# Performance work log

Measured on AMD Instinct MI355X. Metric: run time of the kernel, lower is better.

Reference implementation:

```python
import jax, jax.numpy as jnp
import numpy as np

# Config mirrors cfg['cluster'] and point_cloud_range from init_kwargs
PCR = np.array([-51.2, -51.2, -5.0, 51.2, 51.2, 3.0], dtype=np.float32)
VOXEL_SIZE = 0.2
SIZE_X = 512  # floor((51.2 - (-51.2)) / 0.2)
EPS = 1.5
MIN_SAMPLES = 5
MIN_P_CLUSTER = 20


def _cluster(points):
    """Faithful jax version of Cluster.forward for batch_size == 1.

    voxel_down_sample -> DBSCAN (euclidean, eps, min_samples) on voxel coords
    -> drop clusters with < MIN_P_CLUSTER voxels -> scatter labels back to points.
    """
    N = points.shape[0]
    # --- voxel_down_sample ---
    coords = jnp.floor((points[:, 1:3] - PCR[:2]) / VOXEL_SIZE).astype(jnp.int32)  # (N,2) x,y
    merged = coords[:, 1] * SIZE_X + coords[:, 0]
    # static-size unique: padded entries get fill_value=-1 at the end
    uniq, inv = jnp.unique(merged, size=N, fill_value=-1, return_inverse=True)
    valid = uniq >= 0  # (N,) real voxels
    vox = jnp.stack([uniq % SIZE_X, uniq // SIZE_X], axis=1).astype(jnp.float32)  # (N,2)

    # --- DBSCAN on voxel coords ---
    d2 = jnp.sum((vox[:, None, :] - vox[None, :, :]) ** 2, axis=-1)  # (N,N)
    adj = (d2 <= EPS * EPS) & valid[:, None] & valid[None, :]  # includes self-edge
    core = (jnp.sum(adj, axis=1) >= MIN_SAMPLES) & valid  # sklearn counts self

    BIG = N  # sentinel > any label
    labels0 = jnp.where(core, jnp.arange(N), BIG)
    adj_core = adj & core[None, :]

    def min_core_neighbor(labels):
        return jnp.min(jnp.where(adj_core, labels[None, :], BIG), axis=1)

    def body(carry):
        labels, _ = carry
        new = jnp.where(core, jnp.minimum(labels, min_core_neighbor(labels)), labels)
        return new, jnp.any(new != labels)

    # min-label propagation = connected components over core-core eps graph
    labels, _ = jax.lax.while_loop(lambda c: c[1], body, (labels0, jnp.array(True)))

    # border points attach to a neighboring core cluster; otherwise noise (-1)
    nb = min_core_neighbor(labels)
    raw = jnp.where(core, labels, jnp.where(valid & (nb < BIG), nb, -1))  # root-id or -1

    # relabel root-ids to consecutive 0..k-1 (sklearn numbering by smallest core idx)
    roots = jnp.unique(raw, size=N, fill_value=BIG)  # sorted; BIG padding at end
    pos = jnp.searchsorted(roots, raw)
    dense = pos - (roots[0] == -1).astype(pos.dtype)
    dense = jnp.where(raw >= 0, dense, -1)

    # drop small clusters (by voxel count), keep remaining ids unchanged
    counts = jnp.zeros(N, jnp.int32).at[jnp.where(dense >= 0, dense, 0)].add(
        jnp.where(dense >= 0, 1, 0))
    keep = counts >= MIN_P_CLUSTER
    final = jnp.where((dense >= 0) & keep[jnp.clip(dense, 0, N - 1)], dense, -1)

    # scatter voxel labels back to points (points_inst_idx has points.dtype, like torch)
    pts_inst = final[inv].astype(points.dtype)
    max_num_inst = jnp.maximum(jnp.max(final) + 1, 0)
    return pts_inst, max_num_inst


def setup_inputs() -> dict:
    key = jax.random.key(0)
    N = 8192
    k1, k2, k3, k4, k5, k6, k7 = jax.random.split(key, 7)
    n_blobs = 64
    centers = jax.random.uniform(k1, (n_blobs, 2), minval=-48.0, maxval=48.0)
    assign = jax.random.randint(k2, (N,), 0, n_blobs)
    xy = centers[assign] + jax.random.normal(k3, (N, 2)) * 1.0
    noise = jax.random.uniform(k4, (N,)) < 0.2
    xy = jnp.where(noise[:, None], jax.random.uniform(k5, (N, 2), minval=-51.0, maxval=51.0), xy)
    xy = jnp.clip(xy, -51.0, 51.0)
    z = jax.random.uniform(k6, (N, 1), minval=-3.0, maxval=1.0)
    feat = jax.random.normal(k7, (N, 1))
    points = jnp.concatenate([jnp.zeros((N, 1)), xy, z, feat], axis=1).astype(jnp.float32)
    return {"points": points, "batch_size": 1}


def reference(points, batch_size):
    # voxel_down_sample asserts batch_size == 1; single-batch path.
    return _cluster(points)
```

## Files before the change

### kernel.cpp

```cpp
#include <hip/hip_runtime.h>
#include <stdint.h>


#define GRIDW 512
#define WPR 16
#define NWORDS 8192
#define NCELLS 262144
#define NONE 0xFFFFFFFFu

#define OFF_OCC    0
#define OFF_CNT    8192
#define OFF_ROOTBM 16384
#define OFF_KEEPBM 16640
#define OFF_CM     16896
#define OFF_LAB    25088
#define OFF_PRE    33280
#define OFF_RPRE   41472

__device__ __forceinline__ void hsum(uint32_t l, uint32_t c, uint32_t r,
                                     uint32_t& h0, uint32_t& h1) {
  uint32_t Wb = (c << 1) | (l >> 31);
  uint32_t Eb = (c >> 1) | (r << 31);
  h0 = Wb ^ c ^ Eb;
  h1 = (Wb & c) | (Eb & (Wb ^ c));
}

__device__ __forceinline__ uint32_t ge5(uint32_t a0, uint32_t a1, uint32_t b0,
                                        uint32_t b1, uint32_t c0, uint32_t c1) {
  uint32_t u0 = a0 ^ b0, cy = a0 & b0;
  uint32_t t = a1 ^ b1;
  uint32_t u1 = t ^ cy;
  uint32_t u2 = (a1 & b1) | (cy & t);
  uint32_t v0 = u0 ^ c0, k0 = u0 & c0;
  uint32_t t2 = u1 ^ c1;
  uint32_t v1 = t2 ^ k0;
  uint32_t k1 = (u1 & c1) | (k0 & t2);
  uint32_t v2 = u2 ^ k1;
  uint32_t v3 = u2 & k1;
  return v3 | (v2 & (v1 | v0));
}

__device__ __forceinline__ uint32_t aread(uint32_t* p) {
  return __hip_atomic_load(p, __ATOMIC_RELAXED, __HIP_MEMORY_SCOPE_AGENT);
}

__device__ __forceinline__ uint32_t findc(uint32_t* L, uint32_t x) {
  uint32_t r = x, p = aread(&L[r]);
  while (p != r) { r = p; p = aread(&L[r]); }
  while (x > r) {
    uint32_t nx = aread(&L[x]);
    if (nx <= r) break;
    atomicCAS(&L[x], nx, r);
    x = nx;
  }
  return r;
}

__device__ __forceinline__ void unite(uint32_t* L, uint32_t a, uint32_t b) {
  for (;;) {
    a = findc(L, a);
    b = findc(L, b);
    if (a == b) return;
    uint32_t lo = min(a, b), hi = max(a, b);
    if (atomicCAS(&L[hi], hi, lo) == hi) return;
    a = lo; b = hi;
  }
}

__global__ void k_vox(const float* __restrict__ pts, uint32_t* __restrict__ ws,
                      int npts) {
  int i = blockIdx.x * 256 + threadIdx.x;
  if (i >= npts) return;
  float x = pts[i * 5 + 1];
  float y = pts[i * 5 + 2];
  int cx = (int)floorf((x - (-51.2f)) / 0.2f);
  int cy = (int)floorf((y - (-51.2f)) / 0.2f);
  cx = min(max(cx, 0), GRIDW - 1);
  cy = min(max(cy, 0), GRIDW - 1);
  int cell = cy * GRIDW + cx;
  atomicOr(&ws[OFF_OCC + (cell >> 5)], 1u << (cell & 31));
}

__global__ void k_scan_cm(uint32_t* __restrict__ ws) {
  const uint32_t* occ = ws + OFF_OCC;
  int tid = threadIdx.x;
  if (blockIdx.x == 0) {
    __shared__ uint32_t wsum[4];
    ws[OFF_ROOTBM + tid] = 0u;
    ws[OFF_KEEPBM + tid] = 0u;
    int base = tid * 32;
    uint32_t s = 0;
    for (int j = 0; j < 32; j++) s += __popc(occ[base + j]);
    int lane = tid & 63, wv = tid >> 6;
    uint32_t inc = s;
    for (int d = 1; d < 64; d <<= 1) { uint32_t t = __shfl_up(inc, d); if (lane >= d) inc += t; }
    if (lane == 63) wsum[wv] = inc;
    __syncthreads();
    uint32_t woff = 0;
    for (int k = 0; k < wv; k++) woff += wsum[k];
    uint32_t excl = woff + inc - s;
    uint32_t* pre = ws + OFF_PRE;
    for (int j = 0; j < 32; j++) { pre[base + j] = excl; excl += __popc(occ[base + j]); }
  } else {
    int wi = (blockIdx.x - 1) * 256 + tid;
    ws[OFF_LAB + wi] = (uint32_t)wi;
    ws[OFF_CNT + wi] = 0u;
    uint32_t cB = occ[wi];
    int y = wi >> 4, wx = wi & 15;
    uint32_t lB = wx ? occ[wi - 1] : 0u;
    uint32_t rB = (wx < 15) ? occ[wi + 1] : 0u;
    uint32_t cA = 0, lA = 0, rA = 0, cC = 0, lC = 0, rC = 0;
    if (y > 0) { int wa = wi - WPR; cA = occ[wa]; lA = wx ? occ[wa - 1] : 0u; rA = (wx < 15) ? occ[wa + 1] : 0u; }
    if (y < GRIDW - 1) { int wc = wi + WPR; cC = occ[wc]; lC = wx ? occ[wc - 1] : 0u; rC = (wx < 15) ? occ[wc + 1] : 0u; }
    uint32_t a0, a1, b0, b1, c0, c1;
    hsum(lA, cA, rA, a0, a1); hsum(lB, cB, rB, b0, b1); hsum(lC, cC, rC, c0, c1);
    ws[OFF_CM + wi] = ge5(a0, a1, b0, b1, c0, c1) & cB;
  }
}

__global__ void k_merge(uint32_t* __restrict__ ws) {
  int cell = blockIdx.x * 256 + threadIdx.x;
  const uint32_t* occ = ws + OFF_OCC;
  const uint32_t* cm = ws + OFF_CM;
  const uint32_t* pre = ws + OFF_PRE;
  uint32_t* lab = ws + OFF_LAB;
  int wi = cell >> 5, b = cell & 31, wx = wi & 15;
  uint32_t cw = cm[wi];
  if (!((cw >> b) & 1)) return;
  int y = cell >> 9;
  uint32_t cB = occ[wi];
  int r = pre[wi] + __popc(cB & ((1u << b) - 1u));
  bool eC = (b < 31) ? ((cw >> (b + 1)) & 1) : ((wx < 15) ? (cm[wi + 1] & 1) : false);
  if (eC) unite(lab, r, (b < 31) ? r + 1 : pre[wi + 1]);
  if (y < GRIDW - 1) {
    uint32_t cmS = cm[wi + WPR];
    uint32_t occS = occ[wi + WPR];
    int rS = pre[wi + WPR];
    if ((cmS >> b) & 1) unite(lab, r, rS + __popc(occS & ((1u << b) - 1u)));
    bool seC = (b < 31) ? ((cmS >> (b + 1)) & 1) : ((wx < 15) ? (cm[wi + WPR + 1] & 1) : false);
    if (seC) unite(lab, r, (b < 31) ? rS + __popc(occS & ((2u << b) - 1u)) : pre[wi + WPR + 1]);
    bool swC = (b > 0) ? ((cmS >> (b - 1)) & 1) : ((wx > 0) ? (cm[wi + WPR - 1] >> 31) : false);
    if (swC) unite(lab, r, (b > 0) ? rS + __popc(occS & ((1u << (b - 1)) - 1u)) : rS - 1);
  }
}

__global__ void k_cb(uint32_t* __restrict__ ws) {
  int cell = blockIdx.x * 256 + threadIdx.x;
  int wi = cell >> 5, b = cell & 31, wx = wi & 15;
  const uint32_t* occ = ws + OFF_OCC;
  uint32_t cB = occ[wi];
  if (!((cB >> b) & 1)) return;
  const uint32_t* cm = ws + OFF_CM;
  const uint32_t* pre = ws + OFF_PRE;
  uint32_t* lab = ws + OFF_LAB;
  uint32_t* cnt = ws + OFF_CNT;
  int y = cell >> 9;
  uint32_t cw = cm[wi];
  int r = pre[wi] + __popc(cB & ((1u << b) - 1u));
  if ((cw >> b) & 1) {
    uint32_t root = findc(lab, r);
    lab[r] = root;
    if (root == (uint32_t)r) atomicOr(&ws[OFF_ROOTBM + (r >> 5)], 1u << (r & 31));
    atomicAdd(&cnt[root], 1u);
  } else {
    uint32_t m = NONE;
    bool wC = (b > 0) ? ((cw >> (b - 1)) & 1) : ((wx > 0) ? (cm[wi - 1] >> 31) : false);
    if (wC) m = min(m, findc(lab, (b > 0) ? r - 1 : (int)pre[wi] - 1));
    bool eC = (b < 31) ? ((cw >> (b + 1)) & 1) : ((wx < 15) ? (cm[wi + 1] & 1) : false);
    if (eC) m = min(m, findc(lab, (b < 31) ? r + 1 : pre[wi + 1]));
    if (y > 0) {
      uint32_t cmN = cm[wi - WPR], occN = occ[wi - WPR];
      int rN = pre[wi - WPR];
      if ((cmN >> b) & 1) m = min(m, findc(lab, rN + __popc(occN & ((1u << b) - 1u))));
      bool neC = (b < 31) ? ((cmN >> (b + 1)) & 1) : ((wx < 15) ? (cm[wi - WPR + 1] & 1) : false);
      if (neC) m = min(m, findc(lab, (b < 31) ? rN + __popc(occN & ((2u << b) - 1u)) : pre[wi - WPR + 1]));
      bool nwC = (b > 0) ? ((cmN >> (b - 1)) & 1) : ((wx > 0) ? (cm[wi - WPR - 1] >> 31) : false);
      if (nwC) m = min(m, findc(lab, (b > 0) ? rN + __popc(occN & ((1u << (b - 1)) - 1u)) : rN - 1));
    }
    if (y < GRIDW - 1) {
      uint32_t cmS = cm[wi + WPR], occS = occ[wi + WPR];
      int rS = pre[wi + WPR];
      if ((cmS >> b) & 1) m = min(m, findc(lab, rS + __popc(occS & ((1u << b) - 1u))));
      bool seC = (b < 31) ? ((cmS >> (b + 1)) & 1) : ((wx < 15) ? (cm[wi + WPR + 1] & 1) : false);
      if (seC) m = min(m, findc(lab, (b < 31) ? rS + __popc(occS & ((2u << b) - 1u)) : pre[wi + WPR + 1]));
      bool swC = (b > 0) ? ((cmS >> (b - 1)) & 1) : ((wx > 0) ? (cm[wi + WPR - 1] >> 31) : false);
      if (swC) m = min(m, findc(lab, (b > 0) ? rS + __popc(occS & ((1u << (b - 1)) - 1u)) : rS - 1));
    }
    lab[r] = m;
    if (m != NONE) atomicAdd(&cnt[m], 1u);
  }
}

__global__ void k_finish(uint32_t* __restrict__ ws, float* __restrict__ out,
                         int npts) {
  int tid = threadIdx.x;
  __shared__ uint32_t wsum[4];
  __shared__ int smax;
  if (tid == 0) smax = -1;
  __syncthreads();
  uint32_t rb = ws[OFF_ROOTBM + tid];
  uint32_t v = __popc(rb);
  int lane = tid & 63, wv = tid >> 6;
  uint32_t inc = v;
  for (int d = 1; d < 64; d <<= 1) { uint32_t t = __shfl_up(inc, d); if (lane >= d) inc += t; }
  if (lane == 63) wsum[wv] = inc;
  __syncthreads();
  uint32_t woff = 0;
  for (int k = 0; k < wv; k++) woff += wsum[k];
  uint32_t excl = woff + inc - v;
  ws[OFF_RPRE + tid] = excl;
  uint32_t keep = 0;
  int mx = -1, d = (int)excl;
  while (rb) {
    int b = __ffs(rb) - 1; rb &= rb - 1;
    int r = tid * 32 + b;
    if (ws[OFF_CNT + r] >= 20u) { keep |= 1u << b; mx = d; }
    d++;
  }
  ws[OFF_KEEPBM + tid] = keep;
  if (mx >= 0) atomicMax(&smax, mx);
  __syncthreads();
  if (tid == 0) out[npts] = (float)(smax + 1);
}

__global__ void k_scatter(const float* __restrict__ pts,
                          const uint32_t* __restrict__ ws,
                          float* __restrict__ out, int npts) {
  int i = blockIdx.x * 256 + threadIdx.x;
  if (i >= npts) return;
  float x = pts[i * 5 + 1];
  float y = pts[i * 5 + 2];
  int cx = (int)floorf((x - (-51.2f)) / 0.2f);
  int cy = (int)floorf((y - (-51.2f)) / 0.2f);
  cx = min(max(cx, 0), GRIDW - 1);
  cy = min(max(cy, 0), GRIDW - 1);
  int cell = cy * GRIDW + cx;
  int wi = cell >> 5;
  int r = ws[OFF_PRE + wi] + __popc(ws[OFF_OCC + wi] & ((1u << (cell & 31)) - 1u));
  uint32_t l = ws[OFF_LAB + r];
  float o = -1.0f;
  if (l != NONE && ((ws[OFF_KEEPBM + (l >> 5)] >> (l & 31)) & 1)) {
    int dnum = ws[OFF_RPRE + (l >> 5)] +
               __popc(ws[OFF_ROOTBM + (l >> 5)] & ((1u << (l & 31)) - 1u));
    o = (float)dnum;
  }
  out[i] = o;
}

extern "C" void kernel_launch(void* const* d_in, const int* in_sizes, int n_in,
                              void* d_out, int out_size, void* d_ws, size_t ws_size,
                              hipStream_t stream) {
  const float* pts = (const float*)d_in[0];
  int npts = in_sizes[0] / 5;
  uint32_t* ws = (uint32_t*)d_ws;
  float* out = (float*)d_out;
  int pblocks = (npts + 255) / 256;
  hipMemsetAsync(d_ws, 0, NWORDS * 4, stream);
  k_vox<<<pblocks, 256, 0, stream>>>(pts, ws, npts);
  k_scan_cm<<<33, 256, 0, stream>>>(ws);
  k_merge<<<NCELLS / 256, 256, 0, stream>>>(ws);
  k_cb<<<NCELLS / 256, 256, 0, stream>>>(ws);
  k_finish<<<1, 256, 0, stream>>>(ws, out, npts);
  k_scatter<<<pblocks, 256, 0, stream>>>(pts, ws, out, npts);
}
```

Before: 96.39 us.

## Fuse all clustering stages into one cooperative kernel with grid syncs

Replaces the memset and six separate kernel launches with a single cooperative kernel of 256 blocks that separates the phases (zeroing, voxelization, core mask and prefix scan, union, border attach, finish, scatter) with grid-wide syncs. Each thread now handles a 4-bit nibble of cells instead of one cell per thread, and the prefix scan is spread across blocks followed by a small block-sum scan. The aim is to remove launch and inter-kernel gaps, in exchange for the cost of about eight grid barriers and a cooperative launch.

```diff
diff --git a/kernel.cpp b/kernel.cpp
--- a/kernel.cpp
+++ b/kernel.cpp
@@ -1,21 +1,28 @@
 #include <hip/hip_runtime.h>
+#include <hip/hip_cooperative_groups.h>
 #include <stdint.h>
+
+namespace cg = cooperative_groups;
 
 
 #define GRIDW 512
 #define WPR 16
 #define NWORDS 8192
-#define NCELLS 262144
+#define NB 256
+#define NT 256
+#define TOT (NB * NT)
 #define NONE 0xFFFFFFFFu
 
 #define OFF_OCC    0
 #define OFF_CNT    8192
 #define OFF_ROOTBM 16384
 #define OFF_KEEPBM 16640
-#define OFF_CM     16896
-#define OFF_LAB    25088
-#define OFF_PRE    33280
-#define OFF_RPRE   41472
+#define ZERO_WORDS 16896
+#define OFF_BSUM   16896
+#define OFF_RPRE   17152
+#define OFF_CM     17408
+#define OFF_LAB    25600
+#define OFF_PRE    33792
 
 __device__ __forceinline__ void hsum(uint32_t l, uint32_t c, uint32_t r,
                                      uint32_t& h0, uint32_t& h1) {
@@ -67,184 +74,198 @@
   }
 }
 
-__global__ void k_vox(const float* __restrict__ pts, uint32_t* __restrict__ ws,
-                      int npts) {
-  int i = blockIdx.x * 256 + threadIdx.x;
-  if (i >= npts) return;
-  float x = pts[i * 5 + 1];
-  float y = pts[i * 5 + 2];
-  int cx = (int)floorf((x - (-51.2f)) / 0.2f);
-  int cy = (int)floorf((y - (-51.2f)) / 0.2f);
-  cx = min(max(cx, 0), GRIDW - 1);
-  cy = min(max(cy, 0), GRIDW - 1);
-  int cell = cy * GRIDW + cx;
-  atomicOr(&ws[OFF_OCC + (cell >> 5)], 1u << (cell & 31));
-}
-
-__global__ void k_scan_cm(uint32_t* __restrict__ ws) {
-  const uint32_t* occ = ws + OFF_OCC;
-  int tid = threadIdx.x;
-  if (blockIdx.x == 0) {
-    __shared__ uint32_t wsum[4];
-    ws[OFF_ROOTBM + tid] = 0u;
-    ws[OFF_KEEPBM + tid] = 0u;
-    int base = tid * 32;
-    uint32_t s = 0;
-    for (int j = 0; j < 32; j++) s += __popc(occ[base + j]);
-    int lane = tid & 63, wv = tid >> 6;
-    uint32_t inc = s;
-    for (int d = 1; d < 64; d <<= 1) { uint32_t t = __shfl_up(inc, d); if (lane >= d) inc += t; }
-    if (lane == 63) wsum[wv] = inc;
-    __syncthreads();
-    uint32_t woff = 0;
-    for (int k = 0; k < wv; k++) woff += wsum[k];
-    uint32_t excl = woff + inc - s;
-    uint32_t* pre = ws + OFF_PRE;
-    for (int j = 0; j < 32; j++) { pre[base + j] = excl; excl += __popc(occ[base + j]); }
-  } else {
-    int wi = (blockIdx.x - 1) * 256 + tid;
-    ws[OFF_LAB + wi] = (uint32_t)wi;
-    ws[OFF_CNT + wi] = 0u;
-    uint32_t cB = occ[wi];
-    int y = wi >> 4, wx = wi & 15;
-    uint32_t lB = wx ? occ[wi - 1] : 0u;
-    uint32_t rB = (wx < 15) ? occ[wi + 1] : 0u;
+__global__ __launch_bounds__(NT) void cluster_ck(const float* __restrict__ pts,
+                                                 float* __restrict__ out,
+                                                 uint32_t* __restrict__ ws,
+                                                 int npts) {
+  cg::grid_group grid = cg::this_grid();
+  const int tid = threadIdx.x;
+  const int gid = blockIdx.x * NT + tid;
+  const int lane = tid & 63, wv = tid >> 6;
+  __shared__ uint32_t wsum[4];
+  __shared__ int smax;
+
+  uint32_t* occ = ws + OFF_OCC;
+  uint32_t* cm = ws + OFF_CM;
+  uint32_t* lab = ws + OFF_LAB;
+  uint32_t* pre = ws + OFF_PRE;
+  uint32_t* cnt = ws + OFF_CNT;
+  uint32_t* bsum = ws + OFF_BSUM;
+
+  if (gid < ZERO_WORDS) ws[gid] = 0u;
+  if (gid < NWORDS) lab[gid] = (uint32_t)gid;
+  grid.sync();
+
+  int myCell = -1;
+  if (gid < npts) {
+    float x = pts[gid * 5 + 1];
+    float y = pts[gid * 5 + 2];
+    int cx = (int)floorf((x - (-51.2f)) / 0.2f);
+    int cy = (int)floorf((y - (-51.2f)) / 0.2f);
+    cx = min(max(cx, 0), GRIDW - 1);
+    cy = min(max(cy, 0), GRIDW - 1);
+    myCell = cy * GRIDW + cx;
+    atomicOr(&occ[myCell >> 5], 1u << (myCell & 31));
+  }
+  grid.sync();
+
+  uint32_t s = 0;
+  if (gid < NWORDS) {
+    uint32_t cB = occ[gid];
+    s = __popc(cB);
+    int y = gid >> 4, wx = gid & 15;
+    uint32_t lB = wx ? occ[gid - 1] : 0u;
+    uint32_t rB = (wx < 15) ? occ[gid + 1] : 0u;
     uint32_t cA = 0, lA = 0, rA = 0, cC = 0, lC = 0, rC = 0;
-    if (y > 0) { int wa = wi - WPR; cA = occ[wa]; lA = wx ? occ[wa - 1] : 0u; rA = (wx < 15) ? occ[wa + 1] : 0u; }
-    if (y < GRIDW - 1) { int wc = wi + WPR; cC = occ[wc]; lC = wx ? occ[wc - 1] : 0u; rC = (wx < 15) ? occ[wc + 1] : 0u; }
+    if (y > 0) { int wa = gid - WPR; cA = occ[wa]; lA = wx ? occ[wa - 1] : 0u; rA = (wx < 15) ? occ[wa + 1] : 0u; }
+    if (y < GRIDW - 1) { int wc = gid + WPR; cC = occ[wc]; lC = wx ? occ[wc - 1] : 0u; rC = (wx < 15) ? occ[wc + 1] : 0u; }
     uint32_t a0, a1, b0, b1, c0, c1;
     hsum(lA, cA, rA, a0, a1); hsum(lB, cB, rB, b0, b1); hsum(lC, cC, rC, c0, c1);
-    ws[OFF_CM + wi] = ge5(a0, a1, b0, b1, c0, c1) & cB;
-  }
-}
-
-__global__ void k_merge(uint32_t* __restrict__ ws) {
-  int cell = blockIdx.x * 256 + threadIdx.x;
-  const uint32_t* occ = ws + OFF_OCC;
-  const uint32_t* cm = ws + OFF_CM;
-  const uint32_t* pre = ws + OFF_PRE;
-  uint32_t* lab = ws + OFF_LAB;
-  int wi = cell >> 5, b = cell & 31, wx = wi & 15;
-  uint32_t cw = cm[wi];
-  if (!((cw >> b) & 1)) return;
-  int y = cell >> 9;
-  uint32_t cB = occ[wi];
-  int r = pre[wi] + __popc(cB & ((1u << b) - 1u));
-  bool eC = (b < 31) ? ((cw >> (b + 1)) & 1) : ((wx < 15) ? (cm[wi + 1] & 1) : false);
-  if (eC) unite(lab, r, (b < 31) ? r + 1 : pre[wi + 1]);
-  if (y < GRIDW - 1) {
-    uint32_t cmS = cm[wi + WPR];
-    uint32_t occS = occ[wi + WPR];
-    int rS = pre[wi + WPR];
-    if ((cmS >> b) & 1) unite(lab, r, rS + __popc(occS & ((1u << b) - 1u)));
-    bool seC = (b < 31) ? ((cmS >> (b + 1)) & 1) : ((wx < 15) ? (cm[wi + WPR + 1] & 1) : false);
-    if (seC) unite(lab, r, (b < 31) ? rS + __popc(occS & ((2u << b) - 1u)) : pre[wi + WPR + 1]);
-    bool swC = (b > 0) ? ((cmS >> (b - 1)) & 1) : ((wx > 0) ? (cm[wi + WPR - 1] >> 31) : false);
-    if (swC) unite(lab, r, (b > 0) ? rS + __popc(occS & ((1u << (b - 1)) - 1u)) : rS - 1);
-  }
-}
-
-__global__ void k_cb(uint32_t* __restrict__ ws) {
-  int cell = blockIdx.x * 256 + threadIdx.x;
-  int wi = cell >> 5, b = cell & 31, wx = wi & 15;
-  const uint32_t* occ = ws + OFF_OCC;
-  uint32_t cB = occ[wi];
-  if (!((cB >> b) & 1)) return;
-  const uint32_t* cm = ws + OFF_CM;
-  const uint32_t* pre = ws + OFF_PRE;
-  uint32_t* lab = ws + OFF_LAB;
-  uint32_t* cnt = ws + OFF_CNT;
-  int y = cell >> 9;
-  uint32_t cw = cm[wi];
-  int r = pre[wi] + __popc(cB & ((1u << b) - 1u));
-  if ((cw >> b) & 1) {
-    uint32_t root = findc(lab, r);
-    lab[r] = root;
-    if (root == (uint32_t)r) atomicOr(&ws[OFF_ROOTBM + (r >> 5)], 1u << (r & 31));
-    atomicAdd(&cnt[root], 1u);
-  } else {
-    uint32_t m = NONE;
-    bool wC = (b > 0) ? ((cw >> (b - 1)) & 1) : ((wx > 0) ? (cm[wi - 1] >> 31) : false);
-    if (wC) m = min(m, findc(lab, (b > 0) ? r - 1 : (int)pre[wi] - 1));
-    bool eC = (b < 31) ? ((cw >> (b + 1)) & 1) : ((wx < 15) ? (cm[wi + 1] & 1) : false);
-    if (eC) m = min(m, findc(lab, (b < 31) ? r + 1 : pre[wi + 1]));
-    if (y > 0) {
-      uint32_t cmN = cm[wi - WPR], occN = occ[wi - WPR];
-      int rN = pre[wi - WPR];
-      if ((cmN >> b) & 1) m = min(m, findc(lab, rN + __popc(occN & ((1u << b) - 1u))));
-      bool neC = (b < 31) ? ((cmN >> (b + 1)) & 1) : ((wx < 15) ? (cm[wi - WPR + 1] & 1) : false);
-      if (neC) m = min(m, findc(lab, (b < 31) ? rN + __popc(occN & ((2u << b) - 1u)) : pre[wi - WPR + 1]));
-      bool nwC = (b > 0) ? ((cmN >> (b - 1)) & 1) : ((wx > 0) ? (cm[wi - WPR - 1] >> 31) : false);
-      if (nwC) m = min(m, findc(lab, (b > 0) ? rN + __popc(occN & ((1u << (b - 1)) - 1u)) : rN - 1));
-    }
-    if (y < GRIDW - 1) {
-      uint32_t cmS = cm[wi + WPR], occS = occ[wi + WPR];
-      int rS = pre[wi + WPR];
-      if ((cmS >> b) & 1) m = min(m, findc(lab, rS + __popc(occS & ((1u << b) - 1u))));
-      bool seC = (b < 31) ? ((cmS >> (b + 1)) & 1) : ((wx < 15) ? (cm[wi + WPR + 1] & 1) : false);
-      if (seC) m = min(m, findc(lab, (b < 31) ? rS + __popc(occS & ((2u << b) - 1u)) : pre[wi + WPR + 1]));
-      bool swC = (b > 0) ? ((cmS >> (b - 1)) & 1) : ((wx > 0) ? (cm[wi + WPR - 1] >> 31) : false);
-      if (swC) m = min(m, findc(lab, (b > 0) ? rS + __popc(occS & ((1u << (b - 1)) - 1u)) : rS - 1));
-    }
-    lab[r] = m;
-    if (m != NONE) atomicAdd(&cnt[m], 1u);
-  }
-}
-
-__global__ void k_finish(uint32_t* __restrict__ ws, float* __restrict__ out,
-                         int npts) {
-  int tid = threadIdx.x;
-  __shared__ uint32_t wsum[4];
-  __shared__ int smax;
-  if (tid == 0) smax = -1;
-  __syncthreads();
-  uint32_t rb = ws[OFF_ROOTBM + tid];
-  uint32_t v = __popc(rb);
-  int lane = tid & 63, wv = tid >> 6;
-  uint32_t inc = v;
+    cm[gid] = ge5(a0, a1, b0, b1, c0, c1) & cB;
+  }
+  uint32_t inc = s;
   for (int d = 1; d < 64; d <<= 1) { uint32_t t = __shfl_up(inc, d); if (lane >= d) inc += t; }
   if (lane == 63) wsum[wv] = inc;
   __syncthreads();
   uint32_t woff = 0;
   for (int k = 0; k < wv; k++) woff += wsum[k];
-  uint32_t excl = woff + inc - v;
-  ws[OFF_RPRE + tid] = excl;
-  uint32_t keep = 0;
-  int mx = -1, d = (int)excl;
-  while (rb) {
-    int b = __ffs(rb) - 1; rb &= rb - 1;
-    int r = tid * 32 + b;
-    if (ws[OFF_CNT + r] >= 20u) { keep |= 1u << b; mx = d; }
-    d++;
-  }
-  ws[OFF_KEEPBM + tid] = keep;
-  if (mx >= 0) atomicMax(&smax, mx);
-  __syncthreads();
-  if (tid == 0) out[npts] = (float)(smax + 1);
-}
-
-__global__ void k_scatter(const float* __restrict__ pts,
-                          const uint32_t* __restrict__ ws,
-                          float* __restrict__ out, int npts) {
-  int i = blockIdx.x * 256 + threadIdx.x;
-  if (i >= npts) return;
-  float x = pts[i * 5 + 1];
-  float y = pts[i * 5 + 2];
-  int cx = (int)floorf((x - (-51.2f)) / 0.2f);
-  int cy = (int)floorf((y - (-51.2f)) / 0.2f);
-  cx = min(max(cx, 0), GRIDW - 1);
-  cy = min(max(cy, 0), GRIDW - 1);
-  int cell = cy * GRIDW + cx;
-  int wi = cell >> 5;
-  int r = ws[OFF_PRE + wi] + __popc(ws[OFF_OCC + wi] & ((1u << (cell & 31)) - 1u));
-  uint32_t l = ws[OFF_LAB + r];
-  float o = -1.0f;
-  if (l != NONE && ((ws[OFF_KEEPBM + (l >> 5)] >> (l & 31)) & 1)) {
-    int dnum = ws[OFF_RPRE + (l >> 5)] +
-               __popc(ws[OFF_ROOTBM + (l >> 5)] & ((1u << (l & 31)) - 1u));
-    o = (float)dnum;
-  }
-  out[i] = o;
+  uint32_t binc = woff + inc;
+  if (tid == NT - 1) bsum[blockIdx.x] = binc;
+  grid.sync();
+
+  if (blockIdx.x == 0 && tid < 32) {
+    uint32_t u = bsum[tid];
+    for (int d = 1; d < 32; d <<= 1) { uint32_t t = __shfl_up(u, d); if (tid >= d) u += t; }
+    bsum[tid] = u;
+  }
+  grid.sync();
+
+  if (gid < NWORDS) {
+    uint32_t off = blockIdx.x ? bsum[blockIdx.x - 1] : 0u;
+    pre[gid] = off + binc - s;
+  }
+  grid.sync();
+
+  {
+    int wi = gid >> 3;
+    uint32_t cw = cm[wi];
+    uint32_t nib = (cw >> ((gid & 7) << 2)) & 0xFu;
+    if (nib) {
+      int wx = wi & 15, y = wi >> 4;
+      uint32_t cB = occ[wi];
+      int rbase = pre[wi];
+      bool hasS = y < GRIDW - 1;
+      uint32_t cmS = hasS ? cm[wi + WPR] : 0u;
+      uint32_t occS = hasS ? occ[wi + WPR] : 0u;
+      int rS = hasS ? (int)pre[wi + WPR] : 0;
+      for (int j = 0; j < 4; j++) {
+        int b = ((gid & 7) << 2) + j;
+        if (!((cw >> b) & 1)) continue;
+        int r = rbase + __popc(cB & ((1u << b) - 1u));
+        bool eC = (b < 31) ? ((cw >> (b + 1)) & 1) : ((wx < 15) ? (cm[wi + 1] & 1) : false);
+        if (eC) unite(lab, r, (b < 31) ? r + 1 : pre[wi + 1]);
+        if (hasS) {
+          if ((cmS >> b) & 1) unite(lab, r, rS + __popc(occS & ((1u << b) - 1u)));
+          bool seC = (b < 31) ? ((cmS >> (b + 1)) & 1) : ((wx < 15) ? (cm[wi + WPR + 1] & 1) : false);
+          if (seC) unite(lab, r, (b < 31) ? rS + __popc(occS & ((2u << b) - 1u)) : pre[wi + WPR + 1]);
+          bool swC = (b > 0) ? ((cmS >> (b - 1)) & 1) : ((wx > 0) ? (cm[wi + WPR - 1] >> 31) : false);
+          if (swC) unite(lab, r, (b > 0) ? rS + __popc(occS & ((1u << (b - 1)) - 1u)) : rS - 1);
+        }
+      }
+    }
+  }
+  grid.sync();
+
+  {
+    int wi = gid >> 3;
+    uint32_t cB = occ[wi];
+    uint32_t nib = (cB >> ((gid & 7) << 2)) & 0xFu;
+    if (nib) {
+      int wx = wi & 15, y = wi >> 4;
+      uint32_t cw = cm[wi];
+      int rbase = pre[wi];
+      bool hasN = y > 0, hasS = y < GRIDW - 1;
+      uint32_t cmN = 0, occN = 0, cmS = 0, occS = 0;
+      int rN = 0, rS = 0;
+      if (hasN) { cmN = cm[wi - WPR]; occN = occ[wi - WPR]; rN = pre[wi - WPR]; }
+      if (hasS) { cmS = cm[wi + WPR]; occS = occ[wi + WPR]; rS = pre[wi + WPR]; }
+      for (int j = 0; j < 4; j++) {
+        int b = ((gid & 7) << 2) + j;
+        if (!((cB >> b) & 1)) continue;
+        int r = rbase + __popc(cB & ((1u << b) - 1u));
+        if ((cw >> b) & 1) {
+          uint32_t root = findc(lab, r);
+          lab[r] = root;
+          if (root == (uint32_t)r) atomicOr(&ws[OFF_ROOTBM + (r >> 5)], 1u << (r & 31));
+          atomicAdd(&cnt[root], 1u);
+        } else {
+          uint32_t m = NONE;
+          bool wC = (b > 0) ? ((cw >> (b - 1)) & 1) : ((wx > 0) ? (cm[wi - 1] >> 31) : false);
+          if (wC) m = min(m, findc(lab, (b > 0) ? r - 1 : rbase - 1));
+          bool eC = (b < 31) ? ((cw >> (b + 1)) & 1) : ((wx < 15) ? (cm[wi + 1] & 1) : false);
+          if (eC) m = min(m, findc(lab, (b < 31) ? r + 1 : pre[wi + 1]));
+          if (hasN) {
+            if ((cmN >> b) & 1) m = min(m, findc(lab, rN + __popc(occN & ((1u << b) - 1u))));
+            bool neC = (b < 31) ? ((cmN >> (b + 1)) & 1) : ((wx < 15) ? (cm[wi - WPR + 1] & 1) : false);
+            if (neC) m = min(m, findc(lab, (b < 31) ? rN + __popc(occN & ((2u << b) - 1u)) : pre[wi - WPR + 1]));
+            bool nwC = (b > 0) ? ((cmN >> (b - 1)) & 1) : ((wx > 0) ? (cm[wi - WPR - 1] >> 31) : false);
+            if (nwC) m = min(m, findc(lab, (b > 0) ? rN + __popc(occN & ((1u << (b - 1)) - 1u)) : rN - 1));
+          }
+          if (hasS) {
+            if ((cmS >> b) & 1) m = min(m, findc(lab, rS + __popc(occS & ((1u << b) - 1u))));
+            bool seC = (b < 31) ? ((cmS >> (b + 1)) & 1) : ((wx < 15) ? (cm[wi + WPR + 1] & 1) : false);
+            if (seC) m = min(m, findc(lab, (b < 31) ? rS + __popc(occS & ((2u << b) - 1u)) : pre[wi + WPR + 1]));
+            bool swC = (b > 0) ? ((cmS >> (b - 1)) & 1) : ((wx > 0) ? (cm[wi + WPR - 1] >> 31) : false);
+            if (swC) m = min(m, findc(lab, (b > 0) ? rS + __popc(occS & ((1u << (b - 1)) - 1u)) : rS - 1));
+          }
+          lab[r] = m;
+          if (m != NONE) atomicAdd(&cnt[m], 1u);
+        }
+      }
+    }
+  }
+  grid.sync();
+
+  if (blockIdx.x == 0) {
+    if (tid == 0) smax = -1;
+    __syncthreads();
+    uint32_t rb = ws[OFF_ROOTBM + tid];
+    uint32_t v = __popc(rb);
+    uint32_t rinc = v;
+    for (int d = 1; d < 64; d <<= 1) { uint32_t t = __shfl_up(rinc, d); if (lane >= d) rinc += t; }
+    if (lane == 63) wsum[wv] = rinc;
+    __syncthreads();
+    uint32_t roff = 0;
+    for (int k = 0; k < wv; k++) roff += wsum[k];
+    uint32_t excl = roff + rinc - v;
+    ws[OFF_RPRE + tid] = excl;
+    uint32_t keep = 0;
+    int mx = -1, d = (int)excl;
+    while (rb) {
+      int b = __ffs(rb) - 1; rb &= rb - 1;
+      int r = tid * 32 + b;
+      if (cnt[r] >= 20u) { keep |= 1u << b; mx = d; }
+      d++;
+    }
+    ws[OFF_KEEPBM + tid] = keep;
+    if (mx >= 0) atomicMax(&smax, mx);
+    __syncthreads();
+    if (tid == 0) out[npts] = (float)(smax + 1);
+  }
+  grid.sync();
+
+  if (gid < npts) {
+    int wi = myCell >> 5;
+    int r = pre[wi] + __popc(occ[wi] & ((1u << (myCell & 31)) - 1u));
+    uint32_t l = lab[r];
+    float o = -1.0f;
+    if (l != NONE && ((ws[OFF_KEEPBM + (l >> 5)] >> (l & 31)) & 1)) {
+      int dnum = ws[OFF_RPRE + (l >> 5)] +
+                 __popc(ws[OFF_ROOTBM + (l >> 5)] & ((1u << (l & 31)) - 1u));
+      o = (float)dnum;
+    }
+    out[gid] = o;
+  }
 }
 
 extern "C" void kernel_launch(void* const* d_in, const int* in_sizes, int n_in,
@@ -254,12 +275,7 @@
   int npts = in_sizes[0] / 5;
   uint32_t* ws = (uint32_t*)d_ws;
   float* out = (float*)d_out;
-  int pblocks = (npts + 255) / 256;
-  hipMemsetAsync(d_ws, 0, NWORDS * 4, stream);
-  k_vox<<<pblocks, 256, 0, stream>>>(pts, ws, npts);
-  k_scan_cm<<<33, 256, 0, stream>>>(ws);
-  k_merge<<<NCELLS / 256, 256, 0, stream>>>(ws);
-  k_cb<<<NCELLS / 256, 256, 0, stream>>>(ws);
-  k_finish<<<1, 256, 0, stream>>>(ws, out, npts);
-  k_scatter<<<pblocks, 256, 0, stream>>>(pts, ws, out, npts);
-}
+  void* args[] = {(void*)&pts, (void*)&out, (void*)&ws, (void*)&npts};
+  hipLaunchCooperativeKernel((void*)cluster_ck, dim3(NB), dim3(NT), args, 0,
+                             stream);
+}
```

Result: slower. 305.5 us (+216.9%).

## Index union-find by grid cell and compute core masks inline, dropping scan kernel

Applied to the files above, without the earlier changes.

Switches the label and count arrays from compacted voxel ranks to direct indexing by grid cell (262144 entries). This removes the prefix-sum/core-mask kernel, and core bits are recomputed from the occupancy bitmap inside the merge and border kernels. The root-bitmap scan in the finish kernel grows to 8192 words processed by one block, and a full-size init kernel replaces the small memset. The intent is to remove one launch and the rank-lookup indirection, at the cost of more init traffic, redundant bit arithmetic, and a longer serial scan.

```diff
diff --git a/kernel.cpp b/kernel.cpp
--- a/kernel.cpp
+++ b/kernel.cpp
@@ -9,13 +9,11 @@
 #define NONE 0xFFFFFFFFu
 
 #define OFF_OCC    0
-#define OFF_CNT    8192
-#define OFF_ROOTBM 16384
-#define OFF_KEEPBM 16640
-#define OFF_CM     16896
-#define OFF_LAB    25088
-#define OFF_PRE    33280
-#define OFF_RPRE   41472
+#define OFF_ROOTBM 8192
+#define OFF_KEEPBM 16384
+#define OFF_RPRE   24576
+#define OFF_LAB    32768
+#define OFF_CNT    294912
 
 __device__ __forceinline__ void hsum(uint32_t l, uint32_t c, uint32_t r,
                                      uint32_t& h0, uint32_t& h1) {
@@ -40,6 +38,24 @@
   return v3 | (v2 & (v1 | v0));
 }
 
+__device__ __forceinline__ uint32_t coreRbit(uint32_t cU, uint32_t rU, uint32_t cM,
+                                             uint32_t rM, uint32_t cD, uint32_t rD) {
+  if (!(rM & 1u)) return 0u;
+  int n = __popc((cU >> 31) | ((rU & 3u) << 1)) +
+          __popc((cM >> 31) | ((rM & 3u) << 1)) +
+          __popc((cD >> 31) | ((rD & 3u) << 1));
+  return n >= 5 ? 1u : 0u;
+}
+
+__device__ __forceinline__ uint32_t coreLbit(uint32_t cU, uint32_t lU, uint32_t cM,
+                                             uint32_t lM, uint32_t cD, uint32_t lD) {
+  if (!(lM >> 31)) return 0u;
+  int n = __popc(((lU >> 30) & 3u) | ((cU & 1u) << 2)) +
+          __popc(((lM >> 30) & 3u) | ((cM & 1u) << 2)) +
+          __popc(((lD >> 30) & 3u) | ((cD & 1u) << 2));
+  return n >= 5 ? 1u : 0u;
+}
+
 __device__ __forceinline__ uint32_t aread(uint32_t* p) {
   return __hip_atomic_load(p, __ATOMIC_RELAXED, __HIP_MEMORY_SCOPE_AGENT);
 }
@@ -65,6 +81,13 @@
     if (atomicCAS(&L[hi], hi, lo) == hi) return;
     a = lo; b = hi;
   }
+}
+
+__global__ void k_init(uint32_t* __restrict__ ws) {
+  int i = blockIdx.x * 256 + threadIdx.x;
+  ws[OFF_LAB + i] = (uint32_t)i;
+  ws[OFF_CNT + i] = 0u;
+  if (i < NWORDS) { ws[OFF_OCC + i] = 0u; ws[OFF_ROOTBM + i] = 0u; }
 }
 
 __global__ void k_vox(const float* __restrict__ pts, uint32_t* __restrict__ ws,
@@ -81,143 +104,124 @@
   atomicOr(&ws[OFF_OCC + (cell >> 5)], 1u << (cell & 31));
 }
 
-__global__ void k_scan_cm(uint32_t* __restrict__ ws) {
-  const uint32_t* occ = ws + OFF_OCC;
-  int tid = threadIdx.x;
-  if (blockIdx.x == 0) {
-    __shared__ uint32_t wsum[4];
-    ws[OFF_ROOTBM + tid] = 0u;
-    ws[OFF_KEEPBM + tid] = 0u;
-    int base = tid * 32;
-    uint32_t s = 0;
-    for (int j = 0; j < 32; j++) s += __popc(occ[base + j]);
-    int lane = tid & 63, wv = tid >> 6;
-    uint32_t inc = s;
-    for (int d = 1; d < 64; d <<= 1) { uint32_t t = __shfl_up(inc, d); if (lane >= d) inc += t; }
-    if (lane == 63) wsum[wv] = inc;
-    __syncthreads();
-    uint32_t woff = 0;
-    for (int k = 0; k < wv; k++) woff += wsum[k];
-    uint32_t excl = woff + inc - s;
-    uint32_t* pre = ws + OFF_PRE;
-    for (int j = 0; j < 32; j++) { pre[base + j] = excl; excl += __popc(occ[base + j]); }
-  } else {
-    int wi = (blockIdx.x - 1) * 256 + tid;
-    ws[OFF_LAB + wi] = (uint32_t)wi;
-    ws[OFF_CNT + wi] = 0u;
-    uint32_t cB = occ[wi];
-    int y = wi >> 4, wx = wi & 15;
-    uint32_t lB = wx ? occ[wi - 1] : 0u;
-    uint32_t rB = (wx < 15) ? occ[wi + 1] : 0u;
-    uint32_t cA = 0, lA = 0, rA = 0, cC = 0, lC = 0, rC = 0;
-    if (y > 0) { int wa = wi - WPR; cA = occ[wa]; lA = wx ? occ[wa - 1] : 0u; rA = (wx < 15) ? occ[wa + 1] : 0u; }
-    if (y < GRIDW - 1) { int wc = wi + WPR; cC = occ[wc]; lC = wx ? occ[wc - 1] : 0u; rC = (wx < 15) ? occ[wc + 1] : 0u; }
-    uint32_t a0, a1, b0, b1, c0, c1;
-    hsum(lA, cA, rA, a0, a1); hsum(lB, cB, rB, b0, b1); hsum(lC, cC, rC, c0, c1);
-    ws[OFF_CM + wi] = ge5(a0, a1, b0, b1, c0, c1) & cB;
-  }
-}
-
 __global__ void k_merge(uint32_t* __restrict__ ws) {
   int cell = blockIdx.x * 256 + threadIdx.x;
   const uint32_t* occ = ws + OFF_OCC;
-  const uint32_t* cm = ws + OFF_CM;
-  const uint32_t* pre = ws + OFF_PRE;
   uint32_t* lab = ws + OFF_LAB;
-  int wi = cell >> 5, b = cell & 31, wx = wi & 15;
-  uint32_t cw = cm[wi];
-  if (!((cw >> b) & 1)) return;
-  int y = cell >> 9;
+  int wi = cell >> 5, b = cell & 31, wx = wi & 15, y = cell >> 9;
   uint32_t cB = occ[wi];
-  int r = pre[wi] + __popc(cB & ((1u << b) - 1u));
-  bool eC = (b < 31) ? ((cw >> (b + 1)) & 1) : ((wx < 15) ? (cm[wi + 1] & 1) : false);
-  if (eC) unite(lab, r, (b < 31) ? r + 1 : pre[wi + 1]);
+  if (!((cB >> b) & 1)) return;
+  uint32_t lB = wx ? occ[wi - 1] : 0u;
+  uint32_t rB = (wx < 15) ? occ[wi + 1] : 0u;
+  uint32_t cA = 0, lA = 0, rA = 0, cC = 0, lC = 0, rC = 0, cD = 0, lD = 0, rD = 0;
+  if (y > 0) { int w = wi - WPR; cA = occ[w]; lA = wx ? occ[w - 1] : 0u; rA = (wx < 15) ? occ[w + 1] : 0u; }
+  if (y < GRIDW - 1) { int w = wi + WPR; cC = occ[w]; lC = wx ? occ[w - 1] : 0u; rC = (wx < 15) ? occ[w + 1] : 0u; }
+  if (y < GRIDW - 2) { int w = wi + 2 * WPR; cD = occ[w]; lD = wx ? occ[w - 1] : 0u; rD = (wx < 15) ? occ[w + 1] : 0u; }
+  uint32_t hA0, hA1, hB0, hB1, hC0, hC1, hD0, hD1;
+  hsum(lA, cA, rA, hA0, hA1); hsum(lB, cB, rB, hB0, hB1);
+  hsum(lC, cC, rC, hC0, hC1); hsum(lD, cD, rD, hD0, hD1);
+  uint32_t cmB = ge5(hA0, hA1, hB0, hB1, hC0, hC1) & cB;
+  if (!((cmB >> b) & 1)) return;
+  bool eC = (b < 31) ? (((cmB >> (b + 1)) & 1) != 0)
+                     : (coreRbit(cA, rA, cB, rB, cC, rC) != 0);
+  if (eC) unite(lab, cell, cell + 1);
   if (y < GRIDW - 1) {
-    uint32_t cmS = cm[wi + WPR];
-    uint32_t occS = occ[wi + WPR];
-    int rS = pre[wi + WPR];
-    if ((cmS >> b) & 1) unite(lab, r, rS + __popc(occS & ((1u << b) - 1u)));
-    bool seC = (b < 31) ? ((cmS >> (b + 1)) & 1) : ((wx < 15) ? (cm[wi + WPR + 1] & 1) : false);
-    if (seC) unite(lab, r, (b < 31) ? rS + __popc(occS & ((2u << b) - 1u)) : pre[wi + WPR + 1]);
-    bool swC = (b > 0) ? ((cmS >> (b - 1)) & 1) : ((wx > 0) ? (cm[wi + WPR - 1] >> 31) : false);
-    if (swC) unite(lab, r, (b > 0) ? rS + __popc(occS & ((1u << (b - 1)) - 1u)) : rS - 1);
+    uint32_t cmS = ge5(hB0, hB1, hC0, hC1, hD0, hD1) & cC;
+    if ((cmS >> b) & 1) unite(lab, cell, cell + GRIDW);
+    bool seC = (b < 31) ? (((cmS >> (b + 1)) & 1) != 0)
+                        : (coreRbit(cB, rB, cC, rC, cD, rD) != 0);
+    if (seC) unite(lab, cell, cell + GRIDW + 1);
+    bool swC = (b > 0) ? (((cmS >> (b - 1)) & 1) != 0)
+                       : (coreLbit(cB, lB, cC, lC, cD, lD) != 0);
+    if (swC) unite(lab, cell, cell + GRIDW - 1);
   }
 }
 
 __global__ void k_cb(uint32_t* __restrict__ ws) {
   int cell = blockIdx.x * 256 + threadIdx.x;
-  int wi = cell >> 5, b = cell & 31, wx = wi & 15;
   const uint32_t* occ = ws + OFF_OCC;
+  uint32_t* lab = ws + OFF_LAB;
+  uint32_t* cnt = ws + OFF_CNT;
+  int wi = cell >> 5, b = cell & 31, wx = wi & 15, y = cell >> 9;
   uint32_t cB = occ[wi];
   if (!((cB >> b) & 1)) return;
-  const uint32_t* cm = ws + OFF_CM;
-  const uint32_t* pre = ws + OFF_PRE;
-  uint32_t* lab = ws + OFF_LAB;
-  uint32_t* cnt = ws + OFF_CNT;
-  int y = cell >> 9;
-  uint32_t cw = cm[wi];
-  int r = pre[wi] + __popc(cB & ((1u << b) - 1u));
-  if ((cw >> b) & 1) {
-    uint32_t root = findc(lab, r);
-    lab[r] = root;
-    if (root == (uint32_t)r) atomicOr(&ws[OFF_ROOTBM + (r >> 5)], 1u << (r & 31));
+  uint32_t lB = wx ? occ[wi - 1] : 0u;
+  uint32_t rB = (wx < 15) ? occ[wi + 1] : 0u;
+  uint32_t cZ = 0, lZ = 0, rZ = 0, cA = 0, lA = 0, rA = 0;
+  uint32_t cC = 0, lC = 0, rC = 0, cD = 0, lD = 0, rD = 0;
+  if (y > 1) { int w = wi - 2 * WPR; cZ = occ[w]; lZ = wx ? occ[w - 1] : 0u; rZ = (wx < 15) ? occ[w + 1] : 0u; }
+  if (y > 0) { int w = wi - WPR; cA = occ[w]; lA = wx ? occ[w - 1] : 0u; rA = (wx < 15) ? occ[w + 1] : 0u; }
+  if (y < GRIDW - 1) { int w = wi + WPR; cC = occ[w]; lC = wx ? occ[w - 1] : 0u; rC = (wx < 15) ? occ[w + 1] : 0u; }
+  if (y < GRIDW - 2) { int w = wi + 2 * WPR; cD = occ[w]; lD = wx ? occ[w - 1] : 0u; rD = (wx < 15) ? occ[w + 1] : 0u; }
+  uint32_t hZ0, hZ1, hA0, hA1, hB0, hB1, hC0, hC1, hD0, hD1;
+  hsum(lZ, cZ, rZ, hZ0, hZ1); hsum(lA, cA, rA, hA0, hA1); hsum(lB, cB, rB, hB0, hB1);
+  hsum(lC, cC, rC, hC0, hC1); hsum(lD, cD, rD, hD0, hD1);
+  uint32_t cw0 = ge5(hA0, hA1, hB0, hB1, hC0, hC1) & cB;
+  if ((cw0 >> b) & 1) {
+    uint32_t root = findc(lab, cell);
+    lab[cell] = root;
+    if (root == (uint32_t)cell) atomicOr(&ws[OFF_ROOTBM + wi], 1u << b);
     atomicAdd(&cnt[root], 1u);
   } else {
+    uint32_t cwm1 = ge5(hZ0, hZ1, hA0, hA1, hB0, hB1) & cA;
+    uint32_t cw1 = ge5(hB0, hB1, hC0, hC1, hD0, hD1) & cC;
     uint32_t m = NONE;
-    bool wC = (b > 0) ? ((cw >> (b - 1)) & 1) : ((wx > 0) ? (cm[wi - 1] >> 31) : false);
-    if (wC) m = min(m, findc(lab, (b > 0) ? r - 1 : (int)pre[wi] - 1));
-    bool eC = (b < 31) ? ((cw >> (b + 1)) & 1) : ((wx < 15) ? (cm[wi + 1] & 1) : false);
-    if (eC) m = min(m, findc(lab, (b < 31) ? r + 1 : pre[wi + 1]));
+    bool t;
+    t = (b > 0) ? (((cw0 >> (b - 1)) & 1) != 0) : (coreLbit(cA, lA, cB, lB, cC, lC) != 0);
+    if (t) m = min(m, findc(lab, cell - 1));
+    t = (b < 31) ? (((cw0 >> (b + 1)) & 1) != 0) : (coreRbit(cA, rA, cB, rB, cC, rC) != 0);
+    if (t) m = min(m, findc(lab, cell + 1));
     if (y > 0) {
-      uint32_t cmN = cm[wi - WPR], occN = occ[wi - WPR];
-      int rN = pre[wi - WPR];
-      if ((cmN >> b) & 1) m = min(m, findc(lab, rN + __popc(occN & ((1u << b) - 1u))));
-      bool neC = (b < 31) ? ((cmN >> (b + 1)) & 1) : ((wx < 15) ? (cm[wi - WPR + 1] & 1) : false);
-      if (neC) m = min(m, findc(lab, (b < 31) ? rN + __popc(occN & ((2u << b) - 1u)) : pre[wi - WPR + 1]));
-      bool nwC = (b > 0) ? ((cmN >> (b - 1)) & 1) : ((wx > 0) ? (cm[wi - WPR - 1] >> 31) : false);
-      if (nwC) m = min(m, findc(lab, (b > 0) ? rN + __popc(occN & ((1u << (b - 1)) - 1u)) : rN - 1));
+      if ((cwm1 >> b) & 1) m = min(m, findc(lab, cell - GRIDW));
+      t = (b > 0) ? (((cwm1 >> (b - 1)) & 1) != 0) : (coreLbit(cZ, lZ, cA, lA, cB, lB) != 0);
+      if (t) m = min(m, findc(lab, cell - GRIDW - 1));
+      t = (b < 31) ? (((cwm1 >> (b + 1)) & 1) != 0) : (coreRbit(cZ, rZ, cA, rA, cB, rB) != 0);
+      if (t) m = min(m, findc(lab, cell - GRIDW + 1));
     }
     if (y < GRIDW - 1) {
-      uint32_t cmS = cm[wi + WPR], occS = occ[wi + WPR];
-      int rS = pre[wi + WPR];
-      if ((cmS >> b) & 1) m = min(m, findc(lab, rS + __popc(occS & ((1u << b) - 1u))));
-      bool seC = (b < 31) ? ((cmS >> (b + 1)) & 1) : ((wx < 15) ? (cm[wi + WPR + 1] & 1) : false);
-      if (seC) m = min(m, findc(lab, (b < 31) ? rS + __popc(occS & ((2u << b) - 1u)) : pre[wi + WPR + 1]));
-      bool swC = (b > 0) ? ((cmS >> (b - 1)) & 1) : ((wx > 0) ? (cm[wi + WPR - 1] >> 31) : false);
-      if (swC) m = min(m, findc(lab, (b > 0) ? rS + __popc(occS & ((1u << (b - 1)) - 1u)) : rS - 1));
-    }
-    lab[r] = m;
+      if ((cw1 >> b) & 1) m = min(m, findc(lab, cell + GRIDW));
+      t = (b > 0) ? (((cw1 >> (b - 1)) & 1) != 0) : (coreLbit(cB, lB, cC, lC, cD, lD) != 0);
+      if (t) m = min(m, findc(lab, cell + GRIDW - 1));
+      t = (b < 31) ? (((cw1 >> (b + 1)) & 1) != 0) : (coreRbit(cB, rB, cC, rC, cD, rD) != 0);
+      if (t) m = min(m, findc(lab, cell + GRIDW + 1));
+    }
+    lab[cell] = m;
     if (m != NONE) atomicAdd(&cnt[m], 1u);
   }
 }
 
 __global__ void k_finish(uint32_t* __restrict__ ws, float* __restrict__ out,
                          int npts) {
-  int tid = threadIdx.x;
   __shared__ uint32_t wsum[4];
   __shared__ int smax;
+  int tid = threadIdx.x;
   if (tid == 0) smax = -1;
-  __syncthreads();
-  uint32_t rb = ws[OFF_ROOTBM + tid];
-  uint32_t v = __popc(rb);
+  int base = tid * 32;
+  uint32_t s = 0;
+  for (int j = 0; j < 32; j++) s += __popc(ws[OFF_ROOTBM + base + j]);
   int lane = tid & 63, wv = tid >> 6;
-  uint32_t inc = v;
+  uint32_t inc = s;
   for (int d = 1; d < 64; d <<= 1) { uint32_t t = __shfl_up(inc, d); if (lane >= d) inc += t; }
   if (lane == 63) wsum[wv] = inc;
   __syncthreads();
   uint32_t woff = 0;
   for (int k = 0; k < wv; k++) woff += wsum[k];
-  uint32_t excl = woff + inc - v;
-  ws[OFF_RPRE + tid] = excl;
-  uint32_t keep = 0;
-  int mx = -1, d = (int)excl;
-  while (rb) {
-    int b = __ffs(rb) - 1; rb &= rb - 1;
-    int r = tid * 32 + b;
-    if (ws[OFF_CNT + r] >= 20u) { keep |= 1u << b; mx = d; }
-    d++;
-  }
-  ws[OFF_KEEPBM + tid] = keep;
+  uint32_t excl = woff + inc - s;
+  int mx = -1;
+  for (int j = 0; j < 32; j++) {
+    uint32_t rbw = ws[OFF_ROOTBM + base + j];
+    ws[OFF_RPRE + base + j] = excl;
+    uint32_t rb = rbw, keep = 0;
+    int d = (int)excl;
+    while (rb) {
+      int b2 = __ffs(rb) - 1; rb &= rb - 1;
+      int r = (base + j) * 32 + b2;
+      if (ws[OFF_CNT + r] >= 20u) { keep |= 1u << b2; mx = d; }
+      d++;
+    }
+    ws[OFF_KEEPBM + base + j] = keep;
+    excl += __popc(rbw);
+  }
   if (mx >= 0) atomicMax(&smax, mx);
   __syncthreads();
   if (tid == 0) out[npts] = (float)(smax + 1);
@@ -235,14 +239,14 @@
   cx = min(max(cx, 0), GRIDW - 1);
   cy = min(max(cy, 0), GRIDW - 1);
   int cell = cy * GRIDW + cx;
-  int wi = cell >> 5;
-  int r = ws[OFF_PRE + wi] + __popc(ws[OFF_OCC + wi] & ((1u << (cell & 31)) - 1u));
-  uint32_t l = ws[OFF_LAB + r];
+  uint32_t l = ws[OFF_LAB + cell];
   float o = -1.0f;
-  if (l != NONE && ((ws[OFF_KEEPBM + (l >> 5)] >> (l & 31)) & 1)) {
-    int dnum = ws[OFF_RPRE + (l >> 5)] +
-               __popc(ws[OFF_ROOTBM + (l >> 5)] & ((1u << (l & 31)) - 1u));
-    o = (float)dnum;
+  if (l != NONE) {
+    if ((ws[OFF_KEEPBM + (l >> 5)] >> (l & 31)) & 1) {
+      int dnum = ws[OFF_RPRE + (l >> 5)] +
+                 __popc(ws[OFF_ROOTBM + (l >> 5)] & ((1u << (l & 31)) - 1u));
+      o = (float)dnum;
+    }
   }
   out[i] = o;
 }
@@ -255,9 +259,8 @@
   uint32_t* ws = (uint32_t*)d_ws;
   float* out = (float*)d_out;
   int pblocks = (npts + 255) / 256;
-  hipMemsetAsync(d_ws, 0, NWORDS * 4, stream);
+  k_init<<<NCELLS / 256, 256, 0, stream>>>(ws);
   k_vox<<<pblocks, 256, 0, stream>>>(pts, ws, npts);
-  k_scan_cm<<<33, 256, 0, stream>>>(ws);
   k_merge<<<NCELLS / 256, 256, 0, stream>>>(ws);
   k_cb<<<NCELLS / 256, 256, 0, stream>>>(ws);
   k_finish<<<1, 256, 0, stream>>>(ws, out, npts);
```

Result: slower. 113.7 us (+18.0%).
